# Kernel tuning notes

Hardware: AMD Instinct MI355X
Metric: run time of the kernel (lower is better)

## Reference

```python
import jax, jax.numpy as jnp
import numpy as np

C = 256
H = 8
D = C // H
B = 8
Q_PER = 128
KV_PER = 1024
NQ = B * Q_PER
NKV = B * KV_PER
NEG = -10000.0
MASK_EPS = 1e-6
RMS_EPS = float(np.finfo(np.float32).eps)  # torch RMSNorm default eps=None -> finfo eps


def _rms(x, w):
    return x * jax.lax.rsqrt(jnp.mean(x * x, axis=-1, keepdims=True) + RMS_EPS) * w


def _mlp(x, w1, b1, w2, b2):
    h = jax.nn.gelu(x @ w1.T + b1, approximate=False)  # torch nn.GELU is exact
    return h @ w2.T + b2


def _sdpa(qh, kh, vh, mask, scale):
    # qh [H, Nq, D], kh/vh [H, Nk, D], mask [Nq, Nk] additive
    s = jnp.einsum('hqd,hkd->hqk', qh, kh) * scale + mask[None]
    return jnp.einsum('hqk,hkd->hqd', jax.nn.softmax(s, axis=-1), vh)


def _heads(x):
    return x.reshape(-1, H, D).transpose(1, 0, 2)  # [H, N, D]


def setup_inputs() -> dict:
    key = jax.random.key(0)
    ks = jax.random.split(key, 24)
    s = 0.02
    lin = lambda k, o, i: jax.random.normal(k, (o, i), jnp.float32) * s
    inp = {
        'q': jax.random.normal(ks[0], (NQ, C), jnp.float32),
        'kv': jax.random.normal(ks[1], (NKV, C), jnp.float32),
        'cu_seqlens_q': jnp.arange(B + 1, dtype=jnp.int32) * Q_PER,
        'cu_seqlens_kv': jnp.arange(B + 1, dtype=jnp.int32) * KV_PER,
        'w_norm_kv': jnp.ones((C,), jnp.float32),
        'w_norm1': jnp.ones((C,), jnp.float32),
        'w_norm2': jnp.ones((C,), jnp.float32),
        'w_norm3': jnp.ones((C,), jnp.float32),
        'wq_c': lin(ks[2], C, C), 'wk_c': lin(ks[3], C, C), 'wv_c': lin(ks[4], C, C),
        'wo_c': lin(ks[5], C, C), 'bo_c': jnp.zeros((C,), jnp.float32),
        'wq_s': lin(ks[6], C, C), 'wkv_s': lin(ks[7], 2 * C, C),
        'wo_s': lin(ks[8], C, C), 'bo_s': jnp.zeros((C,), jnp.float32),
        'w1_mlp': lin(ks[9], 4 * C, C), 'b1_mlp': jnp.zeros((4 * C,), jnp.float32),
        'w2_mlp': lin(ks[10], C, 4 * C), 'b2_mlp': jnp.zeros((C,), jnp.float32),
        'w1_mask': lin(ks[11], C, C), 'b1_mask': jnp.zeros((C,), jnp.float32),
        'w2_mask': lin(ks[12], C, C), 'b2_mask': jnp.zeros((C,), jnp.float32),
    }
    return inp


def reference(q, kv, cu_seqlens_q, cu_seqlens_kv, w_norm_kv, w_norm1, w_norm2, w_norm3,
              wq_c, wk_c, wv_c, wo_c, bo_c, wq_s, wkv_s, wo_s, bo_s,
              w1_mlp, b1_mlp, w2_mlp, b2_mlp, w1_mask, b1_mask, w2_mask, b2_mask):
    scale = D ** (-0.5)
    nq, nkv = q.shape[0], kv.shape[0]
    # segment id per packed token from cu_seqlens
    seg_q = jnp.searchsorted(cu_seqlens_q, jnp.arange(nq), side='right') - 1
    seg_kv = jnp.searchsorted(cu_seqlens_kv, jnp.arange(nkv), side='right') - 1

    kv_n = _rms(kv, w_norm_kv)

    # mask MLP -> predicted attention mask (logits z), detached log-prob mask
    m_k = _mlp(q, w1_mask, b1_mask, w2_mask, b2_mask)          # [Nq, C]
    z = m_k @ kv_n.T                                           # [Nq, Nkv]
    p_hat = jax.nn.sigmoid(z)
    same = seg_q[:, None] == seg_kv[None, :]
    attn_mask = jnp.where(same, jnp.log(jax.lax.stop_gradient(p_hat) + MASK_EPS), NEG)

    # cross-attention (pre-norm)
    q_n = _rms(q, w_norm1)
    feat = _sdpa(_heads(q_n @ wq_c.T), _heads(kv_n @ wk_c.T), _heads(kv_n @ wv_c.T),
                 attn_mask, scale)
    feat = feat.transpose(1, 0, 2).reshape(-1, C) @ wo_c.T + bo_c
    q = q + feat

    # block-diagonal self-attention over queries
    q_n = _rms(q, w_norm2)
    kv_proj = (q_n @ wkv_s.T).reshape(-1, 2, H, D)
    self_mask = jnp.where(seg_q[:, None] == seg_q[None, :], 0.0, NEG)
    feat = _sdpa(_heads(q_n @ wq_s.T),
                 kv_proj[:, 0].transpose(1, 0, 2), kv_proj[:, 1].transpose(1, 0, 2),
                 self_mask, scale)
    feat = feat.transpose(1, 0, 2).reshape(-1, C) @ wo_s.T + bo_s
    q = q + feat

    # MLP
    q = q + _mlp(_rms(q, w_norm3), w1_mlp, b1_mlp, w2_mlp, b2_mlp)
    return q
```

## Files before the change

### kernel.cpp

```cpp
#include <hip/hip_runtime.h>
#include <math.h>


#define SCALE_ATTN 0.17677669529663687f
#define RMS_EPS 1.1920929e-07f

typedef __attribute__((ext_vector_type(8))) short bh8;
typedef __attribute__((ext_vector_type(4))) float f32x4;

__device__ __forceinline__ float bf2f(unsigned short s) {
  union { float f; unsigned u; } v; v.u = ((unsigned)s) << 16; return v.f;
}
__device__ __forceinline__ unsigned short f2bf(float f) {
  union { float f; unsigned u; } v; v.f = f;
  unsigned r = v.u + 0x7FFFu + ((v.u >> 16) & 1u);
  return (unsigned short)(r >> 16);
}
__device__ __forceinline__ unsigned pack2bf(float a, float b) {
  union { float f; unsigned u; } x, y; x.f = a; y.f = b;
  return ((x.u + 0x8000u) >> 16) | ((y.u + 0x8000u) & 0xFFFF0000u);
}
__device__ __forceinline__ float gelu_exact(float x) {
  return 0.5f * x * (1.0f + erff(x * 0.70710678118654752440f));
}
__device__ __forceinline__ float sum8sq(int4 v) {
  float s = 0.f;
  unsigned u[4] = {(unsigned)v.x, (unsigned)v.y, (unsigned)v.z, (unsigned)v.w};
#pragma unroll
  for (int i = 0; i < 4; ++i) {
    union { float f; unsigned q; } lo, hi;
    lo.q = u[i] << 16;
    hi.q = u[i] & 0xFFFF0000u;
    s += lo.f * lo.f + hi.f * hi.f;
  }
  return s;
}

struct WP { const float* p[12]; };
__global__ __launch_bounds__(256) void k_pre(
    WP wp, unsigned short* __restrict__ wbf, unsigned short* __restrict__ w2t,
    const float* __restrict__ wn1, const float* __restrict__ wn2,
    const float* __restrict__ wn3,
    const float* __restrict__ kv, const float* __restrict__ wnkv,
    const float* __restrict__ b2m, unsigned short* __restrict__ kv_n,
    float* __restrict__ tvec, unsigned short* __restrict__ q_n) {
  int bid = blockIdx.x, tid = threadIdx.x;
  if (bid < 1408) {
    long g = ((long)bid * 256 + tid) * 4;
    const float* src; long l;
    if (g < 327680)       { src = wp.p[g >> 16]; l = g & 65535; }
    else if (g < 458752)  { src = wp.p[5];  l = g - 327680; }
    else if (g < 524288)  { src = wp.p[6];  l = g - 458752; }
    else if (g < 786432)  { src = wp.p[7];  l = g - 524288; }
    else if (g < 1048576) { src = wp.p[8];  l = g - 786432; }
    else if (g < 1114112) { src = wp.p[9];  l = g - 1048576; }
    else if (g < 1179648) { src = wp.p[10]; l = g - 1114112; }
    else                  { src = wp.p[11]; l = g - 1179648; }
    float4 v = *(const float4*)(src + l);
    if (g >= 262144 && g < 458752) {
      int k = (int)(g & 255);
      v.x *= wn2[k]; v.y *= wn2[k + 1]; v.z *= wn2[k + 2]; v.w *= wn2[k + 3];
    } else if (g >= 524288 && g < 786432) {
      int k = (int)(g & 255);
      v.x *= wn3[k]; v.y *= wn3[k + 1]; v.z *= wn3[k + 2]; v.w *= wn3[k + 3];
    }
    ushort4 o;
    o.x = f2bf(v.x); o.y = f2bf(v.y); o.z = f2bf(v.z); o.w = f2bf(v.w);
    *(ushort4*)(wbf + g) = o;
  } else if (bid < 1424) {
    __shared__ float Ts[64][65];
    int t = bid - 1408, ti = t >> 2, tj = t & 3;
    const float* w2src = wp.p[10];
    int rr = tid >> 2;
#pragma unroll
    for (int j = 0; j < 4; ++j) {
      int cc = (tid & 3) * 16 + j * 4;
      float4 v = *(const float4*)(w2src + (long)(ti * 64 + rr) * 256 + tj * 64 + cc);
      Ts[rr][cc] = v.x; Ts[rr][cc + 1] = v.y;
      Ts[rr][cc + 2] = v.z; Ts[rr][cc + 3] = v.w;
    }
    __syncthreads();
#pragma unroll
    for (int j = 0; j < 4; ++j) {
      int kk = (tid & 3) * 16 + j * 4;
      ushort4 o;
      o.x = f2bf(Ts[kk][rr]); o.y = f2bf(Ts[kk + 1][rr]);
      o.z = f2bf(Ts[kk + 2][rr]); o.w = f2bf(Ts[kk + 3][rr]);
      *(ushort4*)(w2t + (long)(tj * 64 + rr) * 256 + ti * 64 + kk) = o;
    }
  } else if (bid < 3472) {
    int row = (bid - 1424) * 4 + (tid >> 6);
    int c4 = (tid & 63) * 4;
    float4 v = *(const float4*)(kv + (long)row * 256 + c4);
    float s = v.x * v.x + v.y * v.y + v.z * v.z + v.w * v.w;
#pragma unroll
    for (int off = 32; off > 0; off >>= 1) s += __shfl_xor(s, off, 64);
    float inv = rsqrtf(s * (1.0f / 256.0f) + RMS_EPS);
    float4 wn = *(const float4*)(wnkv + c4);
    float4 b2 = *(const float4*)(b2m + c4);
    float4 vn;
    vn.x = v.x * inv * wn.x; vn.y = v.y * inv * wn.y;
    vn.z = v.z * inv * wn.z; vn.w = v.w * inv * wn.w;
    ushort4 o;
    o.x = f2bf(vn.x); o.y = f2bf(vn.y); o.z = f2bf(vn.z); o.w = f2bf(vn.w);
    *(ushort4*)(kv_n + (long)row * 256 + c4) = o;
    float s2 = vn.x * b2.x + vn.y * b2.y + vn.z * b2.z + vn.w * b2.w;
#pragma unroll
    for (int off = 32; off > 0; off >>= 1) s2 += __shfl_xor(s2, off, 64);
    if ((tid & 63) == 0) tvec[row] = s2;
  } else {
    int row = (bid - 3472) * 4 + (tid >> 6);
    int c4 = (tid & 63) * 4;
    const float* q = wp.p[11];
    float4 v = *(const float4*)(q + (long)row * 256 + c4);
    float s = v.x * v.x + v.y * v.y + v.z * v.z + v.w * v.w;
#pragma unroll
    for (int off = 32; off > 0; off >>= 1) s += __shfl_xor(s, off, 64);
    float inv = rsqrtf(s * (1.0f / 256.0f) + RMS_EPS);
    float4 wn = *(const float4*)(wn1 + c4);
    ushort4 o;
    o.x = f2bf(v.x * inv * wn.x); o.y = f2bf(v.y * inv * wn.y);
    o.z = f2bf(v.z * inv * wn.z); o.w = f2bf(v.w * inv * wn.w);
    *(ushort4*)(q_n + (long)row * 256 + c4) = o;
  }
}

template <int MT, int KS, int EPI>
__device__ __forceinline__ void gemm_core(
    const unsigned short* __restrict__ A, const unsigned short* __restrict__ W,
    const float* bias, const float* R,
    float* Cf, unsigned short* Cb, unsigned short* Cb2,
    int lda, int ldw, int ldc, int m0, int n0) {
  int tid = threadIdx.x, w = tid >> 6, lane = tid & 63;
  int quad = lane >> 4, c = lane & 15;
  __shared__ __align__(16) unsigned short As[2][MT * 64][40];
  __shared__ __align__(16) unsigned short Ws[2][64][40];
  __shared__ float ssqLds[64];
  f32x4 acc[MT][4];
#pragma unroll
  for (int i = 0; i < MT; ++i)
#pragma unroll
    for (int j = 0; j < 4; ++j) acc[i][j] = (f32x4){0.f, 0.f, 0.f, 0.f};
  int ar = tid >> 2, ak = (tid & 3) * 8;
  float asum = 0.f;
  {
    int4 a0 = *(const int4*)(A + (long)(m0 + ar) * lda + ak);
    int4 a1;
    if (MT == 2) a1 = *(const int4*)(A + (long)(m0 + 64 + ar) * lda + ak);
    int4 wv = *(const int4*)(W + (long)(n0 + ar) * ldw + ak);
    if (EPI == 8) asum += sum8sq(a0);
    *(int4*)&As[0][ar][ak] = a0;
    if (MT == 2) *(int4*)&As[0][64 + ar][ak] = a1;
    *(int4*)&Ws[0][ar][ak] = wv;
  }
  __syncthreads();
#pragma unroll
  for (int i = 0; i < KS; ++i) {
    int cur = i & 1, nxt = cur ^ 1;
    int4 na0, na1, nwv;
    if (i + 1 < KS) {
      int k0 = (i + 1) * 32;
      na0 = *(const int4*)(A + (long)(m0 + ar) * lda + k0 + ak);
      if (MT == 2)
        na1 = *(const int4*)(A + (long)(m0 + 64 + ar) * lda + k0 + ak);
      nwv = *(const int4*)(W + (long)(n0 + ar) * ldw + k0 + ak);
    }
    bh8 af[MT];
#pragma unroll
    for (int mt = 0; mt < MT; ++mt)
      af[mt] = *(const bh8*)&As[cur][w * (16 * MT) + mt * 16 + c][quad * 8];
#pragma unroll
    for (int nt = 0; nt < 4; ++nt) {
      bh8 bf = *(const bh8*)&Ws[cur][nt * 16 + c][quad * 8];
#pragma unroll
      for (int mt = 0; mt < MT; ++mt)
        acc[mt][nt] =
            __builtin_amdgcn_mfma_f32_16x16x32_bf16(af[mt], bf, acc[mt][nt], 0, 0, 0);
    }
    if (i + 1 < KS) {
      if (EPI == 8) asum += sum8sq(na0);
      *(int4*)&As[nxt][ar][ak] = na0;
      if (MT == 2) *(int4*)&As[nxt][64 + ar][ak] = na1;
      *(int4*)&Ws[nxt][ar][ak] = nwv;
      __syncthreads();
    }
  }
  if (EPI == 8) {
    asum += __shfl_xor(asum, 1, 64);
    asum += __shfl_xor(asum, 2, 64);
    if ((tid & 3) == 0) ssqLds[ar] = asum;
    __syncthreads();
  }
#pragma unroll
  for (int mt = 0; mt < MT; ++mt)
#pragma unroll
    for (int nt = 0; nt < 4; ++nt)
#pragma unroll
      for (int r = 0; r < 4; ++r) {
        int lm = w * (16 * MT) + mt * 16 + quad * 4 + r;
        int m = m0 + lm;
        int n = n0 + nt * 16 + c;
        float v = acc[mt][nt][r];
        long ci = (long)m * ldc + n;
        if (EPI == 1) {
          if (bias) v += bias[n];
          Cb[ci] = f2bf(gelu_exact(v));
        } else if (EPI == 5) {
          Cb[ci] = f2bf(v);
        } else if (EPI == 2) {
          if (bias) v += bias[n];
          v += R[ci];
          Cf[ci] = v;
          if (Cb2) Cb2[ci] = f2bf(v);
        } else {
          v *= rsqrtf(ssqLds[lm] * (1.0f / 256.0f) + RMS_EPS);
          if (bias) v += bias[n];
          Cb[ci] = f2bf(gelu_exact(v));
        }
      }
}

template <int MT, int KS, int EPI>
__global__ __launch_bounds__(256) void k_gemm(
    const unsigned short* A, const unsigned short* W,
    const float* bias, const float* R,
    float* Cf, unsigned short* Cb, unsigned short* Cb2,
    int lda, int ldw, int ldc) {
  gemm_core<MT, KS, EPI>(A, W, bias, R, Cf, Cb, Cb2, lda, ldw, ldc,
                         blockIdx.y * (MT * 64), blockIdx.x * 64);
}

struct G4 {
  const unsigned short* A; const unsigned short* W;
  const float* bias; float* Cf; unsigned short* Cb;
  int lda, ldw, ldc, epi, nx, blkStart;
};
struct G4x { G4 g[4]; };
__global__ __launch_bounds__(256) void k_gemm4(G4x d) {
  int z = blockIdx.x;
  int i = 3;
  while (i > 0 && z < d.g[i].blkStart) --i;
  const G4& g = d.g[i];
  int local = z - g.blkStart;
  int by = local / g.nx, bx = local - by * g.nx;
  if (g.epi == 1)
    gemm_core<2, 8, 1>(g.A, g.W, g.bias, nullptr, nullptr, g.Cb, nullptr,
                       g.lda, g.ldw, g.ldc, by * 128, bx * 64);
  else
    gemm_core<2, 8, 5>(g.A, g.W, g.bias, nullptr, nullptr, g.Cb, nullptr,
                       g.lda, g.ldw, g.ldc, by * 128, bx * 64);
}

__global__ __launch_bounds__(256) void k_flash(
    const unsigned short* __restrict__ Qg,
    const unsigned short* __restrict__ KVg,
    const unsigned short* __restrict__ mh,
    const unsigned short* __restrict__ kvw,
    const float* __restrict__ tvec,
    float* __restrict__ partL, float* __restrict__ partO) {
  int split = blockIdx.x, bh = blockIdx.y;
  int b = bh >> 3, h = bh & 7, j0 = split * 128;
  int tid = threadIdx.x;
  int w = tid >> 6, lane = tid & 63, c = lane & 15, quad = lane >> 4;
  __shared__ __align__(16) unsigned short Ks[128][40];
  __shared__ __align__(16) unsigned short Vt[32][136];
  __shared__ __align__(16) unsigned short Pt[128][136];
  __shared__ float tvLds[128];
  const unsigned short* Qz = Qg + (long)(b * 128) * 256 + h * 32;
  const unsigned short* Kz = KVg + ((long)(b * 1024 + j0)) * 512 + h * 32;
  const unsigned short* Vz = Kz + 256;
  if (tid < 128) tvLds[tid] = tvec[b * 1024 + j0 + tid];
  bh8 Bq[2];
#pragma unroll
  for (int nt = 0; nt < 2; ++nt)
    Bq[nt] = *(const bh8*)(Qz + (long)(w * 32 + nt * 16 + c) * 256 + quad * 8);
  {
    int row = tid >> 2, part = tid & 3;
#pragma unroll
    for (int v = 0; v < 2; ++v) {
      int r2 = row + v * 64;
      *(int4*)&Ks[r2][part * 8] = *(const int4*)(Kz + (long)r2 * 512 + part * 8);
      int4 vv = *(const int4*)(Vz + (long)r2 * 512 + part * 8);
      unsigned short tmp[8];
      *(int4*)tmp = vv;
#pragma unroll
      for (int i = 0; i < 8; ++i) Vt[part * 8 + i][r2] = tmp[i];
    }
  }
  const unsigned short* Az = kvw + (long)(b * 1024 + j0) * 256;
  const unsigned short* Bz = mh + (long)(b * 128) * 256;
  f32x4 Z[8][2];
#pragma unroll
  for (int mt = 0; mt < 8; ++mt)
#pragma unroll
    for (int nt = 0; nt < 2; ++nt) Z[mt][nt] = (f32x4){0.f, 0.f, 0.f, 0.f};
#pragma unroll
  for (int k0 = 0; k0 < 256; k0 += 32) {
    bh8 bz[2];
#pragma unroll
    for (int nt = 0; nt < 2; ++nt)
      bz[nt] = *(const bh8*)(Bz + (long)(w * 32 + nt * 16 + c) * 256 + k0 + quad * 8);
#pragma unroll
    for (int mt = 0; mt < 8; ++mt) {
      bh8 az = *(const bh8*)(Az + (long)(mt * 16 + c) * 256 + k0 + quad * 8);
      Z[mt][0] = __builtin_amdgcn_mfma_f32_16x16x32_bf16(az, bz[0], Z[mt][0], 0, 0, 0);
      Z[mt][1] = __builtin_amdgcn_mfma_f32_16x16x32_bf16(az, bz[1], Z[mt][1], 0, 0, 0);
    }
  }
  __syncthreads();
  f32x4 S[8][2];
#pragma unroll
  for (int mt = 0; mt < 8; ++mt)
#pragma unroll
    for (int nt = 0; nt < 2; ++nt) S[mt][nt] = (f32x4){0.f, 0.f, 0.f, 0.f};
#pragma unroll
  for (int mt = 0; mt < 8; ++mt) {
    bh8 aK = *(const bh8*)&Ks[mt * 16 + c][quad * 8];
    S[mt][0] = __builtin_amdgcn_mfma_f32_16x16x32_bf16(aK, Bq[0], S[mt][0], 0, 0, 0);
    S[mt][1] = __builtin_amdgcn_mfma_f32_16x16x32_bf16(aK, Bq[1], S[mt][1], 0, 0, 0);
  }
  float L[2];
#pragma unroll
  for (int nt = 0; nt < 2; ++nt) {
    float rs = 0.f;
#pragma unroll
    for (int mt = 0; mt < 8; ++mt)
#pragma unroll
      for (int r = 0; r < 4; ++r) {
        float zz = Z[mt][nt][r] + tvLds[mt * 16 + quad * 4 + r];
        float p = 1.0f / (1.0f + __expf(-zz)) + 1e-6f;
        float e = __expf(S[mt][nt][r] * SCALE_ATTN) * p;
        S[mt][nt][r] = e;
        rs += e;
      }
    rs += __shfl_xor(rs, 16, 64);
    rs += __shfl_xor(rs, 32, 64);
    L[nt] = rs;
  }
#pragma unroll
  for (int mt = 0; mt < 8; ++mt)
#pragma unroll
    for (int nt = 0; nt < 2; ++nt) {
      uint2 pk;
      pk.x = pack2bf(S[mt][nt][0], S[mt][nt][1]);
      pk.y = pack2bf(S[mt][nt][2], S[mt][nt][3]);
      *(uint2*)&Pt[w * 32 + nt * 16 + c][mt * 16 + quad * 4] = pk;
    }
  __syncthreads();
  f32x4 acc[2][2];
#pragma unroll
  for (int i = 0; i < 2; ++i)
#pragma unroll
    for (int j = 0; j < 2; ++j) acc[i][j] = (f32x4){0.f, 0.f, 0.f, 0.f};
#pragma unroll
  for (int ks = 0; ks < 4; ++ks) {
    bh8 aP0 = *(const bh8*)&Pt[w * 32 + c][ks * 32 + quad * 8];
    bh8 aP1 = *(const bh8*)&Pt[w * 32 + 16 + c][ks * 32 + quad * 8];
    bh8 bV0 = *(const bh8*)&Vt[c][ks * 32 + quad * 8];
    bh8 bV1 = *(const bh8*)&Vt[16 + c][ks * 32 + quad * 8];
    acc[0][0] = __builtin_amdgcn_mfma_f32_16x16x32_bf16(aP0, bV0, acc[0][0], 0, 0, 0);
    acc[0][1] = __builtin_amdgcn_mfma_f32_16x16x32_bf16(aP0, bV1, acc[0][1], 0, 0, 0);
    acc[1][0] = __builtin_amdgcn_mfma_f32_16x16x32_bf16(aP1, bV0, acc[1][0], 0, 0, 0);
    acc[1][1] = __builtin_amdgcn_mfma_f32_16x16x32_bf16(aP1, bV1, acc[1][1], 0, 0, 0);
  }
  if (quad == 0) {
#pragma unroll
    for (int nt = 0; nt < 2; ++nt)
      partL[((long)(bh * 128 + w * 32 + nt * 16 + c)) * 8 + split] = L[nt];
  }
#pragma unroll
  for (int mt = 0; mt < 2; ++mt)
#pragma unroll
    for (int ct = 0; ct < 2; ++ct)
#pragma unroll
      for (int r = 0; r < 4; ++r) {
        int q = w * 32 + mt * 16 + quad * 4 + r;
        partO[(((long)(bh * 128 + q)) * 8 + split) * 32 + ct * 16 + c] =
            acc[mt][ct][r];
      }
}

__global__ __launch_bounds__(256) void k_gemm_cmb(
    const float* __restrict__ partL, const float* __restrict__ partO,
    const unsigned short* __restrict__ W, const float* __restrict__ bias,
    const float* __restrict__ R,
    float* __restrict__ Cf, unsigned short* __restrict__ Cb2) {
  int m0 = blockIdx.y * 64, n0 = blockIdx.x * 64;
  int tid = threadIdx.x, w = tid >> 6, lane = tid & 63;
  int quad = lane >> 4, c = lane & 15;
  __shared__ __align__(16) unsigned short As[2][64][40];
  __shared__ __align__(16) unsigned short Ws[2][64][40];
  __shared__ float Linv[64][8];
  int ar = tid >> 2, ak = (tid & 3) * 8;
  int b = m0 >> 7, q0 = m0 & 127;
  {
#pragma unroll
    for (int t = 0; t < 2; ++t) {
      int e = tid * 2 + t;
      int rr = e >> 3, hh = e & 7;
      const float* pl = partL + ((long)((b * 8 + hh) * 128 + q0 + rr)) * 8;
      float Ls = 0.f;
#pragma unroll
      for (int s = 0; s < 8; ++s) Ls += pl[s];
      Linv[rr][hh] = 1.0f / Ls;
    }
  }
  __syncthreads();
  auto computeA = [&](int i, uint4& pk) {
    const float* po =
        partO + (((long)((b * 8 + i) * 128 + q0 + ar)) * 8) * 32 + ak;
    float o0 = 0, o1 = 0, o2 = 0, o3 = 0, o4 = 0, o5 = 0, o6 = 0, o7 = 0;
#pragma unroll
    for (int s = 0; s < 8; ++s) {
      float4 u = *(const float4*)(po + s * 32);
      float4 v = *(const float4*)(po + s * 32 + 4);
      o0 += u.x; o1 += u.y; o2 += u.z; o3 += u.w;
      o4 += v.x; o5 += v.y; o6 += v.z; o7 += v.w;
    }
    float inv = Linv[ar][i];
    pk.x = pack2bf(o0 * inv, o1 * inv);
    pk.y = pack2bf(o2 * inv, o3 * inv);
    pk.z = pack2bf(o4 * inv, o5 * inv);
    pk.w = pack2bf(o6 * inv, o7 * inv);
  };
  f32x4 acc[4];
#pragma unroll
  for (int j = 0; j < 4; ++j) acc[j] = (f32x4){0.f, 0.f, 0.f, 0.f};
  {
    uint4 pk;
    computeA(0, pk);
    int4 wv = *(const int4*)(W + (long)(n0 + ar) * 256 + ak);
    *(uint4*)&As[0][ar][ak] = pk;
    *(int4*)&Ws[0][ar][ak] = wv;
  }
  __syncthreads();
#pragma unroll
  for (int i = 0; i < 8; ++i) {
    int cur = i & 1, nxt = cur ^ 1;
    uint4 npk;
    int4 nwv;
    if (i + 1 < 8) {
      computeA(i + 1, npk);
      nwv = *(const int4*)(W + (long)(n0 + ar) * 256 + (i + 1) * 32 + ak);
    }
    bh8 af = *(const bh8*)&As[cur][w * 16 + c][quad * 8];
#pragma unroll
    for (int nt = 0; nt < 4; ++nt) {
      bh8 bf = *(const bh8*)&Ws[cur][nt * 16 + c][quad * 8];
      acc[nt] = __builtin_amdgcn_mfma_f32_16x16x32_bf16(af, bf, acc[nt], 0, 0, 0);
    }
    if (i + 1 < 8) {
      *(uint4*)&As[nxt][ar][ak] = npk;
      *(int4*)&Ws[nxt][ar][ak] = nwv;
      __syncthreads();
    }
  }
#pragma unroll
  for (int nt = 0; nt < 4; ++nt)
#pragma unroll
    for (int r = 0; r < 4; ++r) {
      int m = m0 + w * 16 + quad * 4 + r;
      int n = n0 + nt * 16 + c;
      float v = acc[nt][r] + bias[n];
      long ci = (long)m * 256 + n;
      v += R[ci];
      Cf[ci] = v;
      Cb2[ci] = f2bf(v);
    }
}

__global__ __launch_bounds__(256) void k_selfattn(
    const unsigned short* __restrict__ X,
    const unsigned short* __restrict__ Wqkv,
    unsigned short* __restrict__ feat) {
  int z = blockIdx.x, b = z >> 3, h = z & 7;
  int tid = threadIdx.x, w = tid >> 6, lane = tid & 63;
  int c = lane & 15, quad = lane >> 4;
  __shared__ __align__(16) unsigned short Qs[128][40];
  __shared__ __align__(16) unsigned short Ks[128][40];
  __shared__ __align__(16) unsigned short Vt[32][136];
  __shared__ __align__(16) unsigned short Pt[128][136];
  __shared__ float ssqLds[128];
  const unsigned short* Xz = X + (long)(b * 128) * 256;
  int wr[6];
  wr[0] = h * 32;       wr[1] = h * 32 + 16;
  wr[2] = 256 + h * 32; wr[3] = 256 + h * 32 + 16;
  wr[4] = 512 + h * 32; wr[5] = 512 + h * 32 + 16;
  f32x4 acc[2][6];
#pragma unroll
  for (int i = 0; i < 2; ++i)
#pragma unroll
    for (int j = 0; j < 6; ++j) acc[i][j] = (f32x4){0.f, 0.f, 0.f, 0.f};
  float asq[2] = {0.f, 0.f};
#pragma unroll
  for (int k0 = 0; k0 < 256; k0 += 32) {
    bh8 af[2];
#pragma unroll
    for (int mt = 0; mt < 2; ++mt) {
      af[mt] = *(const bh8*)(Xz + (long)(w * 32 + mt * 16 + c) * 256 + k0 + quad * 8);
      asq[mt] += sum8sq(*(int4*)&af[mt]);
    }
#pragma unroll
    for (int nt = 0; nt < 6; ++nt) {
      bh8 wf = *(const bh8*)(Wqkv + (long)(wr[nt] + c) * 256 + k0 + quad * 8);
#pragma unroll
      for (int mt = 0; mt < 2; ++mt)
        acc[mt][nt] =
            __builtin_amdgcn_mfma_f32_16x16x32_bf16(af[mt], wf, acc[mt][nt], 0, 0, 0);
    }
  }
#pragma unroll
  for (int mt = 0; mt < 2; ++mt) {
    float s = asq[mt];
    s += __shfl_xor(s, 16, 64);
    s += __shfl_xor(s, 32, 64);
    if (quad == 0) ssqLds[w * 32 + mt * 16 + c] = s;
  }
#pragma unroll
  for (int mt = 0; mt < 2; ++mt)
#pragma unroll
    for (int r = 0; r < 4; ++r) {
      int tok = w * 32 + mt * 16 + quad * 4 + r;
      float inv = rsqrtf(ssqLds[tok] * (1.0f / 256.0f) + RMS_EPS);
#pragma unroll
      for (int nt = 0; nt < 6; ++nt) {
        unsigned short bv = f2bf(acc[mt][nt][r] * inv);
        if (nt < 2)      Qs[tok][nt * 16 + c] = bv;
        else if (nt < 4) Ks[tok][(nt - 2) * 16 + c] = bv;
        else             Vt[(nt - 4) * 16 + c][tok] = bv;
      }
    }
  __syncthreads();
  bh8 Bq[2];
#pragma unroll
  for (int nt = 0; nt < 2; ++nt)
    Bq[nt] = *(const bh8*)&Qs[w * 32 + nt * 16 + c][quad * 8];
  f32x4 S[8][2];
#pragma unroll
  for (int mt = 0; mt < 8; ++mt)
#pragma unroll
    for (int nt = 0; nt < 2; ++nt) S[mt][nt] = (f32x4){0.f, 0.f, 0.f, 0.f};
#pragma unroll
  for (int mt = 0; mt < 8; ++mt) {
    bh8 aK = *(const bh8*)&Ks[mt * 16 + c][quad * 8];
    S[mt][0] = __builtin_amdgcn_mfma_f32_16x16x32_bf16(aK, Bq[0], S[mt][0], 0, 0, 0);
    S[mt][1] = __builtin_amdgcn_mfma_f32_16x16x32_bf16(aK, Bq[1], S[mt][1], 0, 0, 0);
  }
  float L[2];
#pragma unroll
  for (int nt = 0; nt < 2; ++nt) {
    float rs = 0.f;
#pragma unroll
    for (int mt = 0; mt < 8; ++mt)
#pragma unroll
      for (int r = 0; r < 4; ++r) {
        float e = __expf(S[mt][nt][r] * SCALE_ATTN);
        S[mt][nt][r] = e;
        rs += e;
      }
    rs += __shfl_xor(rs, 16, 64);
    rs += __shfl_xor(rs, 32, 64);
    L[nt] = rs;
  }
#pragma unroll
  for (int mt = 0; mt < 8; ++mt)
#pragma unroll
    for (int nt = 0; nt < 2; ++nt) {
      uint2 pk;
      pk.x = pack2bf(S[mt][nt][0], S[mt][nt][1]);
      pk.y = pack2bf(S[mt][nt][2], S[mt][nt][3]);
      *(uint2*)&Pt[w * 32 + nt * 16 + c][mt * 16 + quad * 4] = pk;
    }
  __syncthreads();
  f32x4 o[2][2];
#pragma unroll
  for (int i = 0; i < 2; ++i)
#pragma unroll
    for (int j = 0; j < 2; ++j) o[i][j] = (f32x4){0.f, 0.f, 0.f, 0.f};
#pragma unroll
  for (int ks = 0; ks < 4; ++ks) {
    bh8 aP0 = *(const bh8*)&Pt[w * 32 + c][ks * 32 + quad * 8];
    bh8 aP1 = *(const bh8*)&Pt[w * 32 + 16 + c][ks * 32 + quad * 8];
    bh8 bV0 = *(const bh8*)&Vt[c][ks * 32 + quad * 8];
    bh8 bV1 = *(const bh8*)&Vt[16 + c][ks * 32 + quad * 8];
    o[0][0] = __builtin_amdgcn_mfma_f32_16x16x32_bf16(aP0, bV0, o[0][0], 0, 0, 0);
    o[0][1] = __builtin_amdgcn_mfma_f32_16x16x32_bf16(aP0, bV1, o[0][1], 0, 0, 0);
    o[1][0] = __builtin_amdgcn_mfma_f32_16x16x32_bf16(aP1, bV0, o[1][0], 0, 0, 0);
    o[1][1] = __builtin_amdgcn_mfma_f32_16x16x32_bf16(aP1, bV1, o[1][1], 0, 0, 0);
  }
  unsigned short* Oz = feat + (long)(b * 128) * 256 + h * 32;
#pragma unroll
  for (int mt = 0; mt < 2; ++mt)
#pragma unroll
    for (int r = 0; r < 4; ++r) {
      float linv = 1.0f / __shfl(L[mt], quad * 4 + r, 64);
      int q = w * 32 + mt * 16 + quad * 4 + r;
      Oz[(long)q * 256 + c] = f2bf(o[mt][0][r] * linv);
      Oz[(long)q * 256 + 16 + c] = f2bf(o[mt][1][r] * linv);
    }
}

extern "C" void kernel_launch(void* const* d_in, const int* in_sizes, int n_in,
                              void* d_out, int out_size, void* d_ws, size_t ws_size,
                              hipStream_t stream) {
  const float* q        = (const float*)d_in[0];
  const float* kv       = (const float*)d_in[1];
  const float* w_norm_kv = (const float*)d_in[4];
  const float* w_norm1  = (const float*)d_in[5];
  const float* w_norm2  = (const float*)d_in[6];
  const float* w_norm3  = (const float*)d_in[7];
  const float* bo_c     = (const float*)d_in[12];
  const float* bo_s     = (const float*)d_in[16];
  const float* b1_mlp   = (const float*)d_in[18];
  const float* b2_mlp   = (const float*)d_in[20];
  const float* b1_mask  = (const float*)d_in[22];
  const float* b2_mask  = (const float*)d_in[24];
  float* out = (float*)d_out;

  unsigned char* W8 = (unsigned char*)d_ws;
  unsigned short* wbf    = (unsigned short*)(W8 + 0);
  unsigned short* w2t    = (unsigned short*)(W8 + 2883584);
  unsigned short* kv_n   = (unsigned short*)(W8 + 3014656);
  unsigned short* q_n    = (unsigned short*)(W8 + 7208960);
  unsigned short* mh     = (unsigned short*)(W8 + 7733248);
  unsigned short* kvw    = (unsigned short*)(W8 + 8257536);
  float*          tvec   = (float*)(W8 + 14548992);
  unsigned short* Qc     = (unsigned short*)(W8 + 14581760);
  unsigned short* KVc    = (unsigned short*)(W8 + 15106048);
  unsigned short* feat   = (unsigned short*)(W8 + 25067520);
  unsigned short* out1_bf = (unsigned short*)(W8 + 25591808);
  unsigned short* out2_bf = (unsigned short*)(W8 + 26116096);
  float*          partL  = (float*)(W8 + 26648832);
  float*          partO  = (float*)(W8 + 26910976);
  unsigned short* hid    = (unsigned short*)(W8 + 35299584);

  unsigned short* wq_c_bf   = wbf;
  unsigned short* wkv_c_bf  = wbf + 65536;
  unsigned short* wo_c_bf   = wbf + 196608;
  unsigned short* wqkv_s_bf = wbf + 262144;
  unsigned short* wo_s_bf   = wbf + 458752;
  unsigned short* w1_mlp_bf = wbf + 524288;
  unsigned short* w2_mlp_bf = wbf + 786432;
  unsigned short* w1_mask_bf = wbf + 1048576;
  unsigned short* q_bf      = wbf + 1179648;

  WP wp;
  wp.p[0] = (const float*)d_in[8];  wp.p[1] = (const float*)d_in[9];
  wp.p[2] = (const float*)d_in[10]; wp.p[3] = (const float*)d_in[11];
  wp.p[4] = (const float*)d_in[13]; wp.p[5] = (const float*)d_in[14];
  wp.p[6] = (const float*)d_in[15]; wp.p[7] = (const float*)d_in[17];
  wp.p[8] = (const float*)d_in[19]; wp.p[9] = (const float*)d_in[21];
  wp.p[10] = (const float*)d_in[23]; wp.p[11] = q;
  k_pre<<<3728, 256, 0, stream>>>(wp, wbf, w2t, w_norm1, w_norm2, w_norm3,
                                  kv, w_norm_kv, b2_mask, kv_n, tvec, q_n);

  G4x d;
  d.g[0] = {q_bf, w1_mask_bf, b1_mask, nullptr, mh, 256, 256, 256, 1, 4, 0};
  d.g[1] = {q_n, wq_c_bf, nullptr, nullptr, Qc, 256, 256, 256, 5, 4, 32};
  d.g[2] = {kv_n, wkv_c_bf, nullptr, nullptr, KVc, 256, 256, 512, 5, 8, 64};
  d.g[3] = {kv_n, w2t, nullptr, nullptr, kvw, 256, 256, 256, 5, 4, 576};
  k_gemm4<<<832, 256, 0, stream>>>(d);

  k_flash<<<dim3(8, 64), 256, 0, stream>>>(Qc, KVc, mh, kvw, tvec,
                                           partL, partO);

  k_gemm_cmb<<<dim3(4, 16), 256, 0, stream>>>(partL, partO, wo_c_bf, bo_c, q,
                                              out, out1_bf);

  k_selfattn<<<64, 256, 0, stream>>>(out1_bf, wqkv_s_bf, feat);

  k_gemm<1, 8, 2><<<dim3(4, 16), 256, 0, stream>>>(
      feat, wo_s_bf, bo_s, out, out, nullptr, out2_bf, 256, 256, 256);

  k_gemm<1, 8, 8><<<dim3(16, 16), 256, 0, stream>>>(
      out2_bf, w1_mlp_bf, b1_mlp, nullptr, nullptr, hid, nullptr, 256, 256, 1024);

  k_gemm<1, 32, 2><<<dim3(4, 16), 256, 0, stream>>>(
      hid, w2_mlp_bf, b2_mlp, out, out, nullptr, nullptr, 1024, 1024, 256);
}
```

Measured before the change: 215.4 us.

## Precompute sigmoid mask once per batch instead of per head in flash

Adds a k_mask kernel that computes the predicted-mask GEMM plus bias and sigmoid once per batch, storing bf16 probabilities in a workspace buffer. The flash kernel then reads these probabilities instead of recomputing the mask logits via MFMA for each of the 8 heads. This removes redundant per-head matmul work and global loads. In exchange it adds an extra kernel launch, a 2 MB intermediate write/read, and bf16 rounding of the mask probability.

```diff
diff --git a/kernel.cpp b/kernel.cpp
--- a/kernel.cpp
+++ b/kernel.cpp
@@ -207,6 +207,9 @@
           Cb[ci] = f2bf(gelu_exact(v));
         } else if (EPI == 5) {
           Cb[ci] = f2bf(v);
+        } else if (EPI == 3) {
+          v += bias[n];
+          Cb[ci] = f2bf(1.0f / (1.0f + __expf(-v)) + 1e-6f);
         } else if (EPI == 2) {
           if (bias) v += bias[n];
           v += R[ci];
@@ -251,12 +254,21 @@
                        g.lda, g.ldw, g.ldc, by * 128, bx * 64);
 }
 
+__global__ __launch_bounds__(256) void k_mask(
+    const unsigned short* __restrict__ mh, const unsigned short* __restrict__ kvw,
+    const float* __restrict__ tvec, unsigned short* __restrict__ maskp) {
+  int item = blockIdx.x;
+  int z = item >> 5, r = item & 31;
+  gemm_core<1, 8, 3>(mh + (long)z * 128 * 256, kvw + (long)z * 1024 * 256,
+                     tvec + (long)z * 1024, nullptr, nullptr,
+                     maskp + (long)z * 128 * 1024, nullptr,
+                     256, 256, 1024, (r >> 4) * 64, (r & 15) * 64);
+}
+
 __global__ __launch_bounds__(256) void k_flash(
     const unsigned short* __restrict__ Qg,
     const unsigned short* __restrict__ KVg,
-    const unsigned short* __restrict__ mh,
-    const unsigned short* __restrict__ kvw,
-    const float* __restrict__ tvec,
+    const unsigned short* __restrict__ maskp,
     float* __restrict__ partL, float* __restrict__ partO) {
   int split = blockIdx.x, bh = blockIdx.y;
   int b = bh >> 3, h = bh & 7, j0 = split * 128;
@@ -265,11 +277,9 @@
   __shared__ __align__(16) unsigned short Ks[128][40];
   __shared__ __align__(16) unsigned short Vt[32][136];
   __shared__ __align__(16) unsigned short Pt[128][136];
-  __shared__ float tvLds[128];
   const unsigned short* Qz = Qg + (long)(b * 128) * 256 + h * 32;
   const unsigned short* Kz = KVg + ((long)(b * 1024 + j0)) * 512 + h * 32;
   const unsigned short* Vz = Kz + 256;
-  if (tid < 128) tvLds[tid] = tvec[b * 1024 + j0 + tid];
   bh8 Bq[2];
 #pragma unroll
   for (int nt = 0; nt < 2; ++nt)
@@ -287,26 +297,6 @@
       for (int i = 0; i < 8; ++i) Vt[part * 8 + i][r2] = tmp[i];
     }
   }
-  const unsigned short* Az = kvw + (long)(b * 1024 + j0) * 256;
-  const unsigned short* Bz = mh + (long)(b * 128) * 256;
-  f32x4 Z[8][2];
-#pragma unroll
-  for (int mt = 0; mt < 8; ++mt)
-#pragma unroll
-    for (int nt = 0; nt < 2; ++nt) Z[mt][nt] = (f32x4){0.f, 0.f, 0.f, 0.f};
-#pragma unroll
-  for (int k0 = 0; k0 < 256; k0 += 32) {
-    bh8 bz[2];
-#pragma unroll
-    for (int nt = 0; nt < 2; ++nt)
-      bz[nt] = *(const bh8*)(Bz + (long)(w * 32 + nt * 16 + c) * 256 + k0 + quad * 8);
-#pragma unroll
-    for (int mt = 0; mt < 8; ++mt) {
-      bh8 az = *(const bh8*)(Az + (long)(mt * 16 + c) * 256 + k0 + quad * 8);
-      Z[mt][0] = __builtin_amdgcn_mfma_f32_16x16x32_bf16(az, bz[0], Z[mt][0], 0, 0, 0);
-      Z[mt][1] = __builtin_amdgcn_mfma_f32_16x16x32_bf16(az, bz[1], Z[mt][1], 0, 0, 0);
-    }
-  }
   __syncthreads();
   f32x4 S[8][2];
 #pragma unroll
@@ -322,17 +312,21 @@
   float L[2];
 #pragma unroll
   for (int nt = 0; nt < 2; ++nt) {
+    const unsigned short* mrow =
+        maskp + ((long)(b * 128 + w * 32 + nt * 16 + c)) * 1024 + j0;
+#pragma unroll
+    for (int mt = 0; mt < 8; ++mt) {
+      uint2 mp = *(const uint2*)(mrow + mt * 16 + quad * 4);
+      S[mt][nt][0] = __expf(S[mt][nt][0] * SCALE_ATTN) * bf2f((unsigned short)mp.x);
+      S[mt][nt][1] = __expf(S[mt][nt][1] * SCALE_ATTN) * bf2f((unsigned short)(mp.x >> 16));
+      S[mt][nt][2] = __expf(S[mt][nt][2] * SCALE_ATTN) * bf2f((unsigned short)mp.y);
+      S[mt][nt][3] = __expf(S[mt][nt][3] * SCALE_ATTN) * bf2f((unsigned short)(mp.y >> 16));
+    }
     float rs = 0.f;
 #pragma unroll
     for (int mt = 0; mt < 8; ++mt)
 #pragma unroll
-      for (int r = 0; r < 4; ++r) {
-        float zz = Z[mt][nt][r] + tvLds[mt * 16 + quad * 4 + r];
-        float p = 1.0f / (1.0f + __expf(-zz)) + 1e-6f;
-        float e = __expf(S[mt][nt][r] * SCALE_ATTN) * p;
-        S[mt][nt][r] = e;
-        rs += e;
-      }
+      for (int r = 0; r < 4; ++r) rs += S[mt][nt][r];
     rs += __shfl_xor(rs, 16, 64);
     rs += __shfl_xor(rs, 32, 64);
     L[nt] = rs;
@@ -393,17 +387,15 @@
   __shared__ float Linv[64][8];
   int ar = tid >> 2, ak = (tid & 3) * 8;
   int b = m0 >> 7, q0 = m0 & 127;
-  {
-#pragma unroll
-    for (int t = 0; t < 2; ++t) {
-      int e = tid * 2 + t;
-      int rr = e >> 3, hh = e & 7;
-      const float* pl = partL + ((long)((b * 8 + hh) * 128 + q0 + rr)) * 8;
-      float Ls = 0.f;
-#pragma unroll
-      for (int s = 0; s < 8; ++s) Ls += pl[s];
-      Linv[rr][hh] = 1.0f / Ls;
-    }
+#pragma unroll
+  for (int t = 0; t < 2; ++t) {
+    int e = tid * 2 + t;
+    int rr = e >> 3, hh = e & 7;
+    const float* pl = partL + ((long)((b * 8 + hh) * 128 + q0 + rr)) * 8;
+    float Ls = 0.f;
+#pragma unroll
+    for (int s = 0; s < 8; ++s) Ls += pl[s];
+    Linv[rr][hh] = 1.0f / Ls;
   }
   __syncthreads();
   auto computeA = [&](int i, uint4& pk) {
@@ -624,6 +616,7 @@
   unsigned short* q_n    = (unsigned short*)(W8 + 7208960);
   unsigned short* mh     = (unsigned short*)(W8 + 7733248);
   unsigned short* kvw    = (unsigned short*)(W8 + 8257536);
+  unsigned short* maskp  = (unsigned short*)(W8 + 12451840);
   float*          tvec   = (float*)(W8 + 14548992);
   unsigned short* Qc     = (unsigned short*)(W8 + 14581760);
   unsigned short* KVc    = (unsigned short*)(W8 + 15106048);
@@ -661,8 +654,9 @@
   d.g[3] = {kv_n, w2t, nullptr, nullptr, kvw, 256, 256, 256, 5, 4, 576};
   k_gemm4<<<832, 256, 0, stream>>>(d);
 
-  k_flash<<<dim3(8, 64), 256, 0, stream>>>(Qc, KVc, mh, kvw, tvec,
-                                           partL, partO);
+  k_mask<<<256, 256, 0, stream>>>(mh, kvw, tvec, maskp);
+
+  k_flash<<<dim3(8, 64), 256, 0, stream>>>(Qc, KVc, maskp, partL, partO);
 
   k_gemm_cmb<<<dim3(4, 16), 256, 0, stream>>>(partL, partO, wo_c_bf, bo_c, q,
                                               out, out1_bf);
```

Result: faster. 200.9 us (-6.7%).
